# Optimization experiments

Hardware: AMD Instinct MI355X
Metric: run time of the kernel (lower is better)

The kernel has to match this reference:

```python
import jax, jax.numpy as jnp
import numpy as np

J = 4
K = 16  # kernel_size
M_ORDER = 4
PAD = K // 2


def _make_filters():
    t = np.linspace(-2.0, 2.0, K)
    z = 1.0 - 1j * t
    psi = (1.0 / z) ** (M_ORDER + 1)
    psi = psi - psi.mean()
    phi = np.exp(-2.0 * t ** 2)
    phi = phi / phi.sum()
    psi = psi / np.linalg.norm(psi) / np.sqrt(2.0)
    phi = phi / np.linalg.norm(phi) / np.sqrt(2.0)
    return (psi.real.astype(np.float32), psi.imag.astype(np.float32),
            phi.astype(np.float32))


def setup_inputs() -> dict:
    key = jax.random.key(0)
    k1, k2 = jax.random.split(key)
    B, T = 32, 524288
    x_real = jax.random.normal(k1, (B, T), dtype=jnp.float32)
    x_imag = jax.random.normal(k2, (B, T), dtype=jnp.float32)
    pr, pi, ph = _make_filters()
    return {
        'x_real': x_real, 'x_imag': x_imag,
        'psi_real': jnp.asarray(pr), 'psi_imag': jnp.asarray(pi),
        'phi': jnp.asarray(ph),
    }


def _conv_same(x, w, L):
    # x: (B, L) real; w: (K,) real. torch F.conv1d = cross-correlation, 'same'-ish
    # padding K//2 gives length L+1, trimmed back to L (as in the torch code).
    y = jax.lax.conv_general_dilated(x[:, None, :], w[None, None, :],
                                     window_strides=(1,),
                                     padding=[(PAD, PAD)])
    return y[:, 0, :L]


def reference(x_real, x_imag, psi_real, psi_imag, phi):
    x = x_real + 1j * x_imag  # complex64
    coefficients = []
    for j in range(J):
        L = x.shape[-1]
        xr, xi = x.real, x.imag
        # low-pass (complex signal * real filter), then decimate by 2
        s = _conv_same(xr, phi, L) + 1j * _conv_same(xi, phi, L)
        coefficients.append(s[..., ::2])
        # complex band-pass conv: (a+bi)*(c+di)
        rr = _conv_same(xr, psi_real, L)
        ri = _conv_same(xr, psi_imag, L)
        ir = _conv_same(xi, psi_real, L)
        ii = _conv_same(xi, psi_imag, L)
        u = (rr - ii) + 1j * (ri + ir)
        # modulus rectifier (cast back to complex, imag = 0)
        w = jnp.abs(u).astype(u.dtype)
        x = w[..., ::2]
        if x.shape[-1] < K:
            break
    return tuple(coefficients)
```

## Files before the change

kernel.cpp:

```cpp
#include <hip/hip_runtime.h>


using f16x2 = __attribute__((ext_vector_type(2))) __fp16;

static __device__ __forceinline__ uint packh2(float a, float b) {
    f16x2 r = __builtin_amdgcn_cvt_pkrtz(a, b);
    return __builtin_bit_cast(uint, r);
}
static __device__ __forceinline__ float dot2(f16x2 f, uint w, float c) {
#if __has_builtin(__builtin_amdgcn_fdot2)
    return __builtin_amdgcn_fdot2(f, __builtin_bit_cast(f16x2, w), c, false);
#else
    f16x2 h = __builtin_bit_cast(f16x2, w);
    return fmaf((float)f.x, (float)h.x, fmaf((float)f.y, (float)h.y, c));
#endif
}

constexpr int K    = 16;
constexpr int S1   = 1024;
constexpr int H1   = 56;
constexpr int NT1  = S1 + 2 * H1;
constexpr int NG1  = NT1 / 4;
constexpr int NPIN = 1144;
constexpr int NLD  = NPIN / 2;
constexpr int NG2  = 140;
constexpr int NG3  = 68;
constexpr int NTH  = 256;

__global__ __launch_bounds__(NTH, 6) void hst_fused_kernel(
    const float* __restrict__ xr, const float* __restrict__ xi,
    const float* __restrict__ psi_r, const float* __restrict__ psi_i,
    const float* __restrict__ phi,
    float* __restrict__ out,
    long o0, long o1, long o2, long o3,
    int L0, int h0, int h1, int h2, int h3)
{
    __shared__ __align__(16) uint REP[NPIN];
    __shared__ __align__(16) uint IMP[NPIN];
    __shared__ __align__(16) uint X1P[572];
    __shared__ __align__(16) uint X2P[284];
    __shared__ __align__(16) uint X3P[136];

    const int tid = threadIdx.x;
    const int gx  = blockIdx.x;
    const int b   = blockIdx.y;
    const int s   = gx * S1;
    const bool edge = (gx == 0) || (gx == (int)gridDim.x - 1);
    const int X0  = 2 * (s - H1) - 8;

    const float* rowr = xr + (size_t)b * (size_t)L0;
    const float* rowi = xi + (size_t)b * (size_t)L0;

    f16x2 FH[8], FR[8], FI[8];
    #pragma unroll
    for (int j = 0; j < 8; ++j) {
        FH[j] = __builtin_amdgcn_cvt_pkrtz(phi[2*j],   phi[2*j+1]);
        FR[j] = __builtin_amdgcn_cvt_pkrtz(psi_r[2*j], psi_r[2*j+1]);
        FI[j] = __builtin_amdgcn_cvt_pkrtz(psi_i[2*j], psi_i[2*j+1]);
    }

    if (!edge) {
        const float4* pr4 = reinterpret_cast<const float4*>(rowr + X0);
        const float4* pi4 = reinterpret_cast<const float4*>(rowi + X0);
        #pragma unroll
        for (int n = 0; n < 3; ++n) {
            const int i = tid + n * NTH;
            if (i < NLD) {
                float4 a = pr4[i];
                float4 c = pi4[i];
                uint2 wa; wa.x = packh2(a.x, a.y); wa.y = packh2(a.z, a.w);
                uint2 wc; wc.x = packh2(c.x, c.y); wc.y = packh2(c.z, c.w);
                *reinterpret_cast<uint2*>(&REP[2*i]) = wa;
                *reinterpret_cast<uint2*>(&IMP[2*i]) = wc;
            }
        }
    } else {
        for (int i = tid; i < NPIN; i += NTH) {
            int g0 = X0 + 2 * i;
            float r0 = (g0   >= 0 && g0   < L0) ? rowr[g0]   : 0.0f;
            float r1 = (g0+1 >= 0 && g0+1 < L0) ? rowr[g0+1] : 0.0f;
            float i0 = (g0   >= 0 && g0   < L0) ? rowi[g0]   : 0.0f;
            float i1 = (g0+1 >= 0 && g0+1 < L0) ? rowi[g0+1] : 0.0f;
            REP[i] = packh2(r0, r1);
            IMP[i] = packh2(i0, i1);
        }
    }
    __syncthreads();

    #pragma unroll
    for (int n = 0; n < 2; ++n) {
        const int g = tid + n * NTH;
        if (g < NG1) {
            const uint4* wp = reinterpret_cast<const uint4*>(&REP[4*g]);
            uint4 a0 = wp[0], a1 = wp[1], a2 = wp[2];
            const uint4* ip = reinterpret_cast<const uint4*>(&IMP[4*g]);
            uint4 c0v = ip[0], c1v = ip[1], c2v = ip[2];
            const uint wr[12] = {a0.x,a0.y,a0.z,a0.w, a1.x,a1.y,a1.z,a1.w, a2.x,a2.y,a2.z,a2.w};
            const uint wi[12] = {c0v.x,c0v.y,c0v.z,c0v.w, c1v.x,c1v.y,c1v.z,c1v.w, c2v.x,c2v.y,c2v.z,c2v.w};

            float phv[4], mag[4];
            #pragma unroll
            for (int r = 0; r < 4; ++r) {
                float sh = 0.f, rr = 0.f, ri = 0.f, ir = 0.f, ii = 0.f;
                #pragma unroll
                for (int j = 0; j < 8; ++j) {
                    sh = dot2(FH[j], wr[r+j], sh);
                    rr = dot2(FR[j], wr[r+j], rr);
                    ri = dot2(FI[j], wr[r+j], ri);
                    ir = dot2(FR[j], wi[r+j], ir);
                    ii = dot2(FI[j], wi[r+j], ii);
                }
                float ur = rr - ii, ui = ri + ir;
                float m2 = sqrtf(fmaf(ur, ur, ui * ui));
                if (edge) {
                    int m = s - H1 + 4*g + r;
                    m2 = (m >= 0 && m < h0) ? m2 : 0.0f;
                }
                mag[r] = m2;
                phv[r] = sh;
            }
            uint2 xp; xp.x = packh2(mag[0], mag[1]); xp.y = packh2(mag[2], mag[3]);
            *reinterpret_cast<uint2*>(&X1P[2*g]) = xp;

            if (g >= H1/4 && g < H1/4 + S1/4) {
                long m0 = (long)s - H1 + 4*g;
                float4 st; st.x = phv[0]; st.y = phv[1]; st.z = phv[2]; st.w = phv[3];
                *reinterpret_cast<float4*>(out + o0 + (long)b * h0 + m0) = st;
            }
        }
    }
    __syncthreads();

    if (tid < NG2) {
        const int g = tid;
        const uint4* wp = reinterpret_cast<const uint4*>(&X1P[4*g]);
        uint4 a0 = wp[0], a1 = wp[1], a2 = wp[2];
        const uint w[12] = {a0.x,a0.y,a0.z,a0.w, a1.x,a1.y,a1.z,a1.w, a2.x,a2.y,a2.z,a2.w};

        float phv[4], mag[4];
        #pragma unroll
        for (int r = 0; r < 4; ++r) {
            float sh = 0.f, ur = 0.f, ui = 0.f;
            #pragma unroll
            for (int j = 0; j < 8; ++j) {
                sh = dot2(FH[j], w[r+j], sh);
                ur = dot2(FR[j], w[r+j], ur);
                ui = dot2(FI[j], w[r+j], ui);
            }
            float m2 = sqrtf(fmaf(ur, ur, ui * ui));
            const int q = s/2 - 24 + 4*g + r;
            if (edge) m2 = (q >= 0 && q < h1) ? m2 : 0.0f;
            mag[r] = m2;
            phv[r] = sh;
        }
        uint2 xp; xp.x = packh2(mag[0], mag[1]); xp.y = packh2(mag[2], mag[3]);
        *reinterpret_cast<uint2*>(&X2P[2*g]) = xp;

        if (g >= 6 && g < 6 + S1/8) {
            long q0 = (long)s/2 - 24 + 4*g;
            float4 st; st.x = phv[0]; st.y = phv[1]; st.z = phv[2]; st.w = phv[3];
            *reinterpret_cast<float4*>(out + o1 + (long)b * h1 + q0) = st;
        }
    }
    __syncthreads();

    if (tid < NG3) {
        const int g = tid;
        const uint4* wp = reinterpret_cast<const uint4*>(&X2P[4*g]);
        uint4 a0 = wp[0], a1 = wp[1], a2 = wp[2];
        const uint w[12] = {a0.x,a0.y,a0.z,a0.w, a1.x,a1.y,a1.z,a1.w, a2.x,a2.y,a2.z,a2.w};

        float phv[4], mag[4];
        #pragma unroll
        for (int r = 0; r < 4; ++r) {
            float sh = 0.f, ur = 0.f, ui = 0.f;
            #pragma unroll
            for (int j = 0; j < 8; ++j) {
                sh = dot2(FH[j], w[r+j], sh);
                ur = dot2(FR[j], w[r+j], ur);
                ui = dot2(FI[j], w[r+j], ui);
            }
            float m2 = sqrtf(fmaf(ur, ur, ui * ui));
            const int p = s/4 - 8 + 4*g + r;
            if (edge) m2 = (p >= 0 && p < h2) ? m2 : 0.0f;
            mag[r] = m2;
            phv[r] = sh;
        }
        uint2 xp; xp.x = packh2(mag[0], mag[1]); xp.y = packh2(mag[2], mag[3]);
        *reinterpret_cast<uint2*>(&X3P[2*g]) = xp;

        if (g >= 2 && g < 2 + S1/16) {
            long p0 = (long)s/4 - 8 + 4*g;
            float4 st; st.x = phv[0]; st.y = phv[1]; st.z = phv[2]; st.w = phv[3];
            *reinterpret_cast<float4*>(out + o2 + (long)b * h2 + p0) = st;
        }
    }
    __syncthreads();

    if (tid < S1/8) {
        float sh = 0.f;
        #pragma unroll
        for (int j = 0; j < 8; ++j)
            sh = dot2(FH[j], X3P[tid + j], sh);
        out[o3 + (long)b * h3 + (s/8 + tid)] = sh;
    }
}

extern "C" void kernel_launch(void* const* d_in, const int* in_sizes, int n_in,
                              void* d_out, int out_size, void* d_ws, size_t ws_size,
                              hipStream_t stream) {
    const float* xr    = (const float*)d_in[0];
    const float* xi    = (const float*)d_in[1];
    const float* psi_r = (const float*)d_in[2];
    const float* psi_i = (const float*)d_in[3];
    const float* phi   = (const float*)d_in[4];
    float* out = (float*)d_out;

    const int B  = 32;
    const int T  = in_sizes[0] / B;
    const int L0 = T;
    const int h0 = L0 / 2;
    const int h1 = h0 / 2;
    const int h2 = h1 / 2;
    const int h3 = h2 / 2;

    const long o0 = 0;
    const long o1 = o0 + (long)B * h0;
    const long o2 = o1 + (long)B * h1;
    const long o3 = o2 + (long)B * h2;

    dim3 blk(NTH, 1, 1);
    dim3 grd(h0 / S1, B, 1);
    hipLaunchKernelGGL(hst_fused_kernel, grd, blk, 0, stream,
                       xr, xi, psi_r, psi_i, phi,
                       out, o0, o1, o2, o3,
                       L0, h0, h1, h2, h3);
}
```

Baseline: 48.35 us.

## Rebalance per-thread work across stages to fill all waves evenly

```diff
diff --git a/kernel.cpp b/kernel.cpp
--- a/kernel.cpp
+++ b/kernel.cpp
@@ -16,15 +16,11 @@
 #endif
 }
 
-constexpr int K    = 16;
 constexpr int S1   = 1024;
 constexpr int H1   = 56;
 constexpr int NT1  = S1 + 2 * H1;
-constexpr int NG1  = NT1 / 4;
 constexpr int NPIN = 1144;
 constexpr int NLD  = NPIN / 2;
-constexpr int NG2  = 140;
-constexpr int NG3  = 68;
 constexpr int NTH  = 256;
 
 __global__ __launch_bounds__(NTH, 6) void hst_fused_kernel(
@@ -41,12 +37,14 @@
     __shared__ __align__(16) uint X2P[284];
     __shared__ __align__(16) uint X3P[136];
 
-    const int tid = threadIdx.x;
-    const int gx  = blockIdx.x;
-    const int b   = blockIdx.y;
-    const int s   = gx * S1;
+    const int tid  = threadIdx.x;
+    const int wv   = tid >> 6;
+    const int lane = tid & 63;
+    const int gx   = blockIdx.x;
+    const int b    = blockIdx.y;
+    const int s    = gx * S1;
     const bool edge = (gx == 0) || (gx == (int)gridDim.x - 1);
-    const int X0  = 2 * (s - H1) - 8;
+    const int X0   = 2 * (s - H1) - 8;
 
     const float* rowr = xr + (size_t)b * (size_t)L0;
     const float* rowi = xi + (size_t)b * (size_t)L0;
@@ -63,8 +61,17 @@
         const float4* pr4 = reinterpret_cast<const float4*>(rowr + X0);
         const float4* pi4 = reinterpret_cast<const float4*>(rowi + X0);
         #pragma unroll
-        for (int n = 0; n < 3; ++n) {
+        for (int n = 0; n < 2; ++n) {
             const int i = tid + n * NTH;
+            float4 a = pr4[i];
+            float4 c = pi4[i];
+            uint2 wa; wa.x = packh2(a.x, a.y); wa.y = packh2(a.z, a.w);
+            uint2 wc; wc.x = packh2(c.x, c.y); wc.y = packh2(c.z, c.w);
+            *reinterpret_cast<uint2*>(&REP[2*i]) = wa;
+            *reinterpret_cast<uint2*>(&IMP[2*i]) = wc;
+        }
+        if (lane < 15) {
+            const int i = 512 + 4 * lane + wv;
             if (i < NLD) {
                 float4 a = pr4[i];
                 float4 c = pi4[i];
@@ -87,59 +94,85 @@
     }
     __syncthreads();
 
-    #pragma unroll
-    for (int n = 0; n < 2; ++n) {
-        const int g = tid + n * NTH;
-        if (g < NG1) {
-            const uint4* wp = reinterpret_cast<const uint4*>(&REP[4*g]);
-            uint4 a0 = wp[0], a1 = wp[1], a2 = wp[2];
-            const uint4* ip = reinterpret_cast<const uint4*>(&IMP[4*g]);
-            uint4 c0v = ip[0], c1v = ip[1], c2v = ip[2];
-            const uint wr[12] = {a0.x,a0.y,a0.z,a0.w, a1.x,a1.y,a1.z,a1.w, a2.x,a2.y,a2.z,a2.w};
-            const uint wi[12] = {c0v.x,c0v.y,c0v.z,c0v.w, c1v.x,c1v.y,c1v.z,c1v.w, c2v.x,c2v.y,c2v.z,c2v.w};
-
-            float phv[4], mag[4];
+    {
+        const int g = tid;
+        const uint4* wp = reinterpret_cast<const uint4*>(&REP[4*g]);
+        uint4 a0 = wp[0], a1 = wp[1], a2 = wp[2];
+        const uint4* ip = reinterpret_cast<const uint4*>(&IMP[4*g]);
+        uint4 c0v = ip[0], c1v = ip[1], c2v = ip[2];
+        const uint wr[12] = {a0.x,a0.y,a0.z,a0.w, a1.x,a1.y,a1.z,a1.w, a2.x,a2.y,a2.z,a2.w};
+        const uint wi[12] = {c0v.x,c0v.y,c0v.z,c0v.w, c1v.x,c1v.y,c1v.z,c1v.w, c2v.x,c2v.y,c2v.z,c2v.w};
+
+        float phv[4], mag[4];
+        #pragma unroll
+        for (int r = 0; r < 4; ++r) {
+            float sh = 0.f, rr = 0.f, ri = 0.f, ir = 0.f, ii = 0.f;
             #pragma unroll
-            for (int r = 0; r < 4; ++r) {
-                float sh = 0.f, rr = 0.f, ri = 0.f, ir = 0.f, ii = 0.f;
-                #pragma unroll
-                for (int j = 0; j < 8; ++j) {
-                    sh = dot2(FH[j], wr[r+j], sh);
-                    rr = dot2(FR[j], wr[r+j], rr);
-                    ri = dot2(FI[j], wr[r+j], ri);
-                    ir = dot2(FR[j], wi[r+j], ir);
-                    ii = dot2(FI[j], wi[r+j], ii);
-                }
-                float ur = rr - ii, ui = ri + ir;
-                float m2 = sqrtf(fmaf(ur, ur, ui * ui));
-                if (edge) {
-                    int m = s - H1 + 4*g + r;
-                    m2 = (m >= 0 && m < h0) ? m2 : 0.0f;
-                }
-                mag[r] = m2;
-                phv[r] = sh;
-            }
-            uint2 xp; xp.x = packh2(mag[0], mag[1]); xp.y = packh2(mag[2], mag[3]);
-            *reinterpret_cast<uint2*>(&X1P[2*g]) = xp;
-
-            if (g >= H1/4 && g < H1/4 + S1/4) {
-                long m0 = (long)s - H1 + 4*g;
-                float4 st; st.x = phv[0]; st.y = phv[1]; st.z = phv[2]; st.w = phv[3];
-                *reinterpret_cast<float4*>(out + o0 + (long)b * h0 + m0) = st;
-            }
-        }
-    }
-    __syncthreads();
-
-    if (tid < NG2) {
-        const int g = tid;
-        const uint4* wp = reinterpret_cast<const uint4*>(&X1P[4*g]);
-        uint4 a0 = wp[0], a1 = wp[1], a2 = wp[2];
-        const uint w[12] = {a0.x,a0.y,a0.z,a0.w, a1.x,a1.y,a1.z,a1.w, a2.x,a2.y,a2.z,a2.w};
-
-        float phv[4], mag[4];
-        #pragma unroll
-        for (int r = 0; r < 4; ++r) {
+            for (int j = 0; j < 8; ++j) {
+                sh = dot2(FH[j], wr[r+j], sh);
+                rr = dot2(FR[j], wr[r+j], rr);
+                ri = dot2(FI[j], wr[r+j], ri);
+                ir = dot2(FR[j], wi[r+j], ir);
+                ii = dot2(FI[j], wi[r+j], ii);
+            }
+            float ur = rr - ii, ui = ri + ir;
+            float m2 = sqrtf(fmaf(ur, ur, ui * ui));
+            if (edge) {
+                int m = s - H1 + 4*g + r;
+                m2 = (m >= 0 && m < h0) ? m2 : 0.0f;
+            }
+            mag[r] = m2;
+            phv[r] = sh;
+        }
+        uint2 xp; xp.x = packh2(mag[0], mag[1]); xp.y = packh2(mag[2], mag[3]);
+        *reinterpret_cast<uint2*>(&X1P[2*g]) = xp;
+
+        if (g >= 14) {
+            long m0 = (long)s - H1 + 4*g;
+            float4 st; st.x = phv[0]; st.y = phv[1]; st.z = phv[2]; st.w = phv[3];
+            *reinterpret_cast<float4*>(out + o0 + (long)b * h0 + m0) = st;
+        }
+    }
+
+    if (lane < 28) {
+        const int h  = 4 * lane + wv;
+        const int lm = 1024 + h;
+        uint wr8[8], wi8[8];
+        #pragma unroll
+        for (int j = 0; j < 8; ++j) { wr8[j] = REP[lm + j]; wi8[j] = IMP[lm + j]; }
+        float sh = 0.f, rr = 0.f, ri = 0.f, ir = 0.f, ii = 0.f;
+        #pragma unroll
+        for (int j = 0; j < 8; ++j) {
+            sh = dot2(FH[j], wr8[j], sh);
+            rr = dot2(FR[j], wr8[j], rr);
+            ri = dot2(FI[j], wr8[j], ri);
+            ir = dot2(FR[j], wi8[j], ir);
+            ii = dot2(FI[j], wi8[j], ii);
+        }
+        float ur = rr - ii, ui = ri + ir;
+        float m2 = sqrtf(fmaf(ur, ur, ui * ui));
+        if (edge) {
+            int m = s - H1 + lm;
+            m2 = (m >= 0 && m < h0) ? m2 : 0.0f;
+        }
+        reinterpret_cast<__fp16*>(X1P)[lm] = (__fp16)m2;
+        if (h < 56)
+            out[o0 + (long)b * h0 + (s + 968 + h)] = sh;
+    }
+    __syncthreads();
+
+    {
+        const int t = tid;
+        uint2 u0 = *reinterpret_cast<const uint2*>(&X1P[2*t]);
+        uint2 u1 = *reinterpret_cast<const uint2*>(&X1P[2*t+2]);
+        uint2 u2 = *reinterpret_cast<const uint2*>(&X1P[2*t+4]);
+        uint2 u3 = *reinterpret_cast<const uint2*>(&X1P[2*t+6]);
+        uint  w8 = X1P[2*t+8];
+        const uint w[9] = {u0.x,u0.y,u1.x,u1.y,u2.x,u2.y,u3.x,u3.y,w8};
+
+        float phv[2], mag[2];
+        #pragma unroll
+        for (int r = 0; r < 2; ++r) {
             float sh = 0.f, ur = 0.f, ui = 0.f;
             #pragma unroll
             for (int j = 0; j < 8; ++j) {
@@ -148,31 +181,52 @@
                 ui = dot2(FI[j], w[r+j], ui);
             }
             float m2 = sqrtf(fmaf(ur, ur, ui * ui));
-            const int q = s/2 - 24 + 4*g + r;
+            const int q = s/2 - 24 + 2*t + r;
             if (edge) m2 = (q >= 0 && q < h1) ? m2 : 0.0f;
             mag[r] = m2;
             phv[r] = sh;
         }
-        uint2 xp; xp.x = packh2(mag[0], mag[1]); xp.y = packh2(mag[2], mag[3]);
-        *reinterpret_cast<uint2*>(&X2P[2*g]) = xp;
-
-        if (g >= 6 && g < 6 + S1/8) {
-            long q0 = (long)s/2 - 24 + 4*g;
-            float4 st; st.x = phv[0]; st.y = phv[1]; st.z = phv[2]; st.w = phv[3];
-            *reinterpret_cast<float4*>(out + o1 + (long)b * h1 + q0) = st;
-        }
-    }
-    __syncthreads();
-
-    if (tid < NG3) {
-        const int g = tid;
-        const uint4* wp = reinterpret_cast<const uint4*>(&X2P[4*g]);
-        uint4 a0 = wp[0], a1 = wp[1], a2 = wp[2];
-        const uint w[12] = {a0.x,a0.y,a0.z,a0.w, a1.x,a1.y,a1.z,a1.w, a2.x,a2.y,a2.z,a2.w};
-
-        float phv[4], mag[4];
-        #pragma unroll
-        for (int r = 0; r < 4; ++r) {
+        X2P[t] = packh2(mag[0], mag[1]);
+        if (t >= 12) {
+            long q0 = (long)s/2 - 24 + 2*t;
+            *reinterpret_cast<float2*>(out + o1 + (long)b * h1 + q0) =
+                make_float2(phv[0], phv[1]);
+        }
+    }
+    if (lane < 12) {
+        const int h   = 4 * lane + wv;
+        const int pos = 512 + h;
+        uint w8[8];
+        #pragma unroll
+        for (int j = 0; j < 8; ++j) w8[j] = X1P[pos + j];
+        float sh = 0.f, ur = 0.f, ui = 0.f;
+        #pragma unroll
+        for (int j = 0; j < 8; ++j) {
+            sh = dot2(FH[j], w8[j], sh);
+            ur = dot2(FR[j], w8[j], ur);
+            ui = dot2(FI[j], w8[j], ui);
+        }
+        float m2 = sqrtf(fmaf(ur, ur, ui * ui));
+        const int q = s/2 - 24 + pos;
+        if (edge) m2 = (q >= 0 && q < h1) ? m2 : 0.0f;
+        reinterpret_cast<__fp16*>(X2P)[pos] = (__fp16)m2;
+        if (h < 24)
+            out[o1 + (long)b * h1 + q] = sh;
+    }
+    __syncthreads();
+
+    if (tid < 136) {
+        const int t = tid;
+        uint2 u0 = *reinterpret_cast<const uint2*>(&X2P[2*t]);
+        uint2 u1 = *reinterpret_cast<const uint2*>(&X2P[2*t+2]);
+        uint2 u2 = *reinterpret_cast<const uint2*>(&X2P[2*t+4]);
+        uint2 u3 = *reinterpret_cast<const uint2*>(&X2P[2*t+6]);
+        uint  w8 = X2P[2*t+8];
+        const uint w[9] = {u0.x,u0.y,u1.x,u1.y,u2.x,u2.y,u3.x,u3.y,w8};
+
+        float phv[2], mag[2];
+        #pragma unroll
+        for (int r = 0; r < 2; ++r) {
             float sh = 0.f, ur = 0.f, ui = 0.f;
             #pragma unroll
             for (int j = 0; j < 8; ++j) {
@@ -181,18 +235,16 @@
                 ui = dot2(FI[j], w[r+j], ui);
             }
             float m2 = sqrtf(fmaf(ur, ur, ui * ui));
-            const int p = s/4 - 8 + 4*g + r;
+            const int p = s/4 - 8 + 2*t + r;
             if (edge) m2 = (p >= 0 && p < h2) ? m2 : 0.0f;
             mag[r] = m2;
             phv[r] = sh;
         }
-        uint2 xp; xp.x = packh2(mag[0], mag[1]); xp.y = packh2(mag[2], mag[3]);
-        *reinterpret_cast<uint2*>(&X3P[2*g]) = xp;
-
-        if (g >= 2 && g < 2 + S1/16) {
-            long p0 = (long)s/4 - 8 + 4*g;
-            float4 st; st.x = phv[0]; st.y = phv[1]; st.z = phv[2]; st.w = phv[3];
-            *reinterpret_cast<float4*>(out + o2 + (long)b * h2 + p0) = st;
+        X3P[t] = packh2(mag[0], mag[1]);
+        if (t >= 4 && t < 132) {
+            long p0 = (long)s/4 - 8 + 2*t;
+            *reinterpret_cast<float2*>(out + o2 + (long)b * h2 + p0) =
+                make_float2(phv[0], phv[1]);
         }
     }
     __syncthreads();
```

Result: slower. 49.32 us (+2.0%).
